# Performance work log

Measured on AMD Instinct MI355X. Metric: run time of the kernel, lower is better.

The kernel has to match this reference:

```python
import jax, jax.numpy as jnp
import numpy as np

EPS = 1e-5  # torch BatchNorm1d default eps
O, T, D, H1, H2 = 8, 4, 256, 64, 32


def setup_inputs() -> dict:
    key = jax.random.key(0)
    ks = jax.random.split(key, 8)
    B = 65536
    feature = jax.random.normal(ks[0], (B, D), dtype=jnp.float32)
    treatment = jax.random.randint(ks[1], (B,), 0, T, dtype=jnp.int64)
    s1 = 1.0 / np.sqrt(D)
    s2 = 1.0 / np.sqrt(H1)
    s3 = 1.0 / np.sqrt(H2)
    params = {
        # per (outcome, treatment) expert MLP weights
        'W1': jax.random.uniform(ks[2], (O, T, D, H1), jnp.float32, -s1, s1),
        'b1': jnp.zeros((O, T, H1), jnp.float32),
        'g1': jnp.ones((O, T, H1), jnp.float32),   # BN1 gamma
        'be1': jnp.zeros((O, T, H1), jnp.float32),  # BN1 beta
        'm1': jnp.zeros((O, T, H1), jnp.float32),   # BN1 running mean
        'v1': jnp.ones((O, T, H1), jnp.float32),    # BN1 running var
        'W2': jax.random.uniform(ks[3], (O, T, H1, H2), jnp.float32, -s2, s2),
        'b2': jnp.zeros((O, T, H2), jnp.float32),
        'g2': jnp.ones((O, T, H2), jnp.float32),
        'be2': jnp.zeros((O, T, H2), jnp.float32),
        'm2': jnp.zeros((O, T, H2), jnp.float32),
        'v2': jnp.ones((O, T, H2), jnp.float32),
        'W3': jax.random.uniform(ks[4], (O, T, H2), jnp.float32, -s3, s3),  # final Linear(32,1), squeezed
        'b3': jnp.zeros((O, T), jnp.float32),
    }
    return {'feature': feature, 'treatment': treatment, **params}


def _tlearner_fwd(x, t, W1, b1, g1, be1, m1, v1, W2, b2, g2, be2, m2, v2, W3, b3):
    # Dense evaluation of every (outcome, treatment) expert, then per-row
    # selection by treatment id. Equivalent (in eval mode: BN uses running
    # stats, dropout off) to the masked dispatch of the original module.
    h = jnp.einsum('bd,otdh->both', x, W1) + b1          # [B,O,T,H1]
    h = jax.nn.relu(h)
    h = (h - m1) * jax.lax.rsqrt(v1 + EPS) * g1 + be1    # BN1 (eval)
    h = jnp.einsum('both,othk->botk', h, W2) + b2        # [B,O,T,H2]
    h = jax.nn.relu(h)
    h = (h - m2) * jax.lax.rsqrt(v2 + EPS) * g2 + be2    # BN2 (eval)
    out = jnp.einsum('botk,otk->bot', h, W3) + b3        # [B,O,T]
    idx = t.astype(jnp.int32)[:, None, None]             # [B,1,1]
    return jnp.take_along_axis(out, jnp.broadcast_to(idx, (out.shape[0], O, 1)), axis=2)[..., 0]  # [B,O]


def reference(feature, treatment, W1, b1, g1, be1, m1, v1, W2, b2, g2, be2, m2, v2, W3, b3):
    return _tlearner_fwd(feature, treatment, W1, b1, g1, be1, m1, v1,
                         W2, b2, g2, be2, m2, v2, W3, b3)
```

## Files before the change

### kernel.cpp

```cpp
#include <hip/hip_runtime.h>
#include <cstdint>

typedef short bf16x8 __attribute__((ext_vector_type(8)));
typedef float f32x4 __attribute__((ext_vector_type(4)));

#define NO 8
#define NT 4
#define ND 256
#define NH1 64
#define NH2 32
#define BM 32
#define BNEPS 1e-5f

__device__ __forceinline__ unsigned bfpack2(float a, float b) {
    unsigned ua = __float_as_uint(a), ub = __float_as_uint(b);
    ua = (ua + 0x7FFFu + ((ua >> 16) & 1u)) >> 16;
    ub = (ub + 0x7FFFu + ((ub >> 16) & 1u)) >> 16;
    return ua | (ub << 16);
}


__global__ void k_hist_prep(const int* __restrict__ trt, int* __restrict__ ws, int B,
                            const float* __restrict__ W1, const float* __restrict__ W2,
                            const float* __restrict__ b1, const float* __restrict__ g1,
                            const float* __restrict__ be1, const float* __restrict__ m1,
                            const float* __restrict__ v1,
                            const float* __restrict__ b2, const float* __restrict__ g2,
                            const float* __restrict__ be2, const float* __restrict__ m2,
                            const float* __restrict__ v2, const float* __restrict__ W3,
                            unsigned* __restrict__ W1T4, unsigned* __restrict__ W2T4,
                            float* __restrict__ P1, float* __restrict__ P2) {
    const int bid = blockIdx.x, tid = threadIdx.x;
    if (bid < 256) {
        __shared__ int loc[NT];
        if (tid < NT) loc[tid] = 0;
        __syncthreads();
        const int i = bid * 256 + tid;
        if (i < B) atomicAdd(&loc[trt[i] & 3], 1);
        __syncthreads();
        if (tid < NT) atomicAdd(&ws[tid], loc[tid]);
    } else if (bid < 512) {
        const int gi = (bid - 256) * 256 + tid;
        const int lane = gi & 63, nt = (gi >> 6) & 31, c = (gi >> 11) & 7, t = gi >> 14;
        const int n16 = lane & 15, kg = lane >> 4;
        const int n = nt * 16 + n16, o = n >> 6, h = n & 63;
        const int k0 = c * 32 + kg * 8;
        const float* src = W1 + ((size_t)(o * NT + t) * ND + k0) * NH1 + h;
        float v[8];
#pragma unroll
        for (int j = 0; j < 8; ++j) v[j] = src[(size_t)j * NH1];
        uint4 q;
        q.x = bfpack2(v[0], v[1]); q.y = bfpack2(v[2], v[3]);
        q.z = bfpack2(v[4], v[5]); q.w = bfpack2(v[6], v[7]);
        ((uint4*)W1T4)[gi] = q;
    } else if (bid < 544) {
        const int gi = (bid - 512) * 256 + tid;
        const int m16 = gi & 15, kg = (gi >> 4) & 3, ks = (gi >> 6) & 1,
                  kt = (gi >> 7) & 1, o = (gi >> 8) & 7, t = gi >> 11;
        const int k2 = kt * 16 + m16, hb = ks * 32 + kg * 8;
        const float* src = W2 + ((size_t)(o * NT + t) * NH1 + hb) * NH2 + k2;
        float v[8];
#pragma unroll
        for (int j = 0; j < 8; ++j) v[j] = src[(size_t)j * NH2];
        uint4 q;
        q.x = bfpack2(v[0], v[1]); q.y = bfpack2(v[2], v[3]);
        q.z = bfpack2(v[4], v[5]); q.w = bfpack2(v[6], v[7]);
        ((uint4*)W2T4)[gi] = q;
    } else if (bid < 552) {
        const int gi = (bid - 544) * 256 + tid;
        const int t = gi >> 9, n = gi & 511;
        const int o = n >> 6, h = n & 63;
        const int idx = (o * NT + t) * NH1 + h;
        const float sc = g1[idx] * rsqrtf(v1[idx] + BNEPS);
        P1[gi] = sc;
        P1[2048 + gi] = be1[idx] - m1[idx] * sc;
        P1[4096 + gi] = b1[idx];
    } else {
        const int gi = (bid - 552) * 256 + tid;
        const int t = gi >> 8, q = gi & 255;
        const int o = q >> 5, k2 = q & 31;
        const int idx = (o * NT + t) * NH2 + k2;
        const float s = g2[idx] * rsqrtf(v2[idx] + BNEPS);
        const float w3 = W3[idx];
        P2[gi] = s * w3;
        P2[1024 + gi] = (be2[idx] - m2[idx] * s) * w3;
        P2[2048 + gi] = b2[idx];
    }
}

__global__ void k_scatter(const int* __restrict__ trt, int* __restrict__ ws,
                          int* __restrict__ perm, int B) {
    __shared__ int loc[NT], gb[NT];
    const int tid = threadIdx.x;
    if (tid < NT) loc[tid] = 0;
    __syncthreads();
    const int i = blockIdx.x * blockDim.x + tid;
    int tt = 0, pos = 0;
    if (i < B) { tt = trt[i] & 3; pos = atomicAdd(&loc[tt], 1); }
    __syncthreads();
    if (tid < NT) {
        const int c0 = ws[0], c1 = ws[1], c2 = ws[2];
        const int ub = tid == 0 ? 0 : tid == 1 ? c0 : tid == 2 ? c0 + c1 : c0 + c1 + c2;
        gb[tid] = ub + atomicAdd(&ws[4 + tid], loc[tid]);
    }
    __syncthreads();
    if (i < B) perm[gb[tt] + pos] = i;
}

__global__ __launch_bounds__(256, 3) void k_main(
    const float* __restrict__ X, const int* __restrict__ ws, const int* __restrict__ perm,
    const char* __restrict__ W1T, const char* __restrict__ W2T,
    const float* __restrict__ P1, const float* __restrict__ P2,
    const float* __restrict__ pb3, float* __restrict__ out)
{
    const int c0 = ws[0], c1 = ws[1], c2 = ws[2], c3 = ws[3];
    const int q0 = (c0 + 31) & ~31, q1 = (c1 + 31) & ~31, q2 = (c2 + 31) & ~31;
    const int e0 = q0, e1 = q0 + q1, e2 = e1 + q2, e3 = e2 + ((c3 + 31) & ~31);
    const int m0 = blockIdx.x * BM;
    if (m0 >= e3) return;
    const int t = (m0 >= e0) + (m0 >= e1) + (m0 >= e2);
    const int pb = t == 0 ? 0 : t == 1 ? e0 : t == 2 ? e1 : e2;
    const int ub = t == 0 ? 0 : t == 1 ? c0 : t == 2 ? c0 + c1 : c0 + c1 + c2;
    const int n_t = t == 0 ? c0 : t == 1 ? c1 : t == 2 ? c2 : c3;
    const int ploc0 = m0 - pb;

    const int tid = threadIdx.x;
    const int w = tid >> 6;
    const int l = tid & 63;

    __shared__ __align__(16) char LDS[32768];

    const int pl = ploc0 + (l & 31);
    const int rid_l = perm[ub + min(pl, n_t - 1)];

#pragma unroll
    for (int j = 0; j < 8; ++j) {
        const int r = w * 8 + j;
        const int rr = __shfl(rid_l, r);
        const float4 xv = *(const float4*)(X + (size_t)rr * ND + l * 4);
        uint2 pk;
        pk.x = bfpack2(xv.x, xv.y);
        pk.y = bfpack2(xv.z, xv.w);
        *(uint2*)(LDS + r * 512 + ((l * 8) ^ ((r & 7) << 4))) = pk;
    }

    f32x4 acc[8][2];
#pragma unroll
    for (int nt = 0; nt < 8; ++nt)
#pragma unroll
        for (int rt = 0; rt < 2; ++rt) acc[nt][rt] = (f32x4){0.f, 0.f, 0.f, 0.f};

    const char* W1Tt = W1T + (size_t)t * 262144;
    const int ln4 = (l >> 4) * 4;

    __syncthreads();

#pragma unroll
    for (int c = 0; c < 8; ++c) {
        bf16x8 aA[8];
#pragma unroll
        for (int nt = 0; nt < 8; ++nt)
            aA[nt] = *(const bf16x8*)(W1Tt + c * 32768 + (w * 8 + nt) * 1024 + l * 16);
#pragma unroll
        for (int rt = 0; rt < 2; ++rt) {
            const int r = rt * 16 + (l & 15);
            const bf16x8 bX = *(const bf16x8*)(LDS + r * 512 +
                                               ((c * 64 + (l >> 4) * 16) ^ ((r & 7) << 4)));
#pragma unroll
            for (int nt = 0; nt < 8; ++nt)
                acc[nt][rt] = __builtin_amdgcn_mfma_f32_16x16x32_bf16(aA[nt], bX, acc[nt][rt], 0, 0, 0);
        }
    }
    __syncthreads();

#pragma unroll
    for (int nt = 0; nt < 8; ++nt) {
        const int n0 = (w * 8 + nt) * 16 + ln4;
        const int p = t * 512 + n0;
        const float4 scv = *(const float4*)(P1 + p);
        const float4 shv = *(const float4*)(P1 + 2048 + p);
        const float4 bbv = *(const float4*)(P1 + 4096 + p);
#pragma unroll
        for (int rt = 0; rt < 2; ++rt) {
            const int r = rt * 16 + (l & 15);
            const f32x4 a = acc[nt][rt];
            const float z0 = fmaf(fmaxf(a[0] + bbv.x, 0.f), scv.x, shv.x);
            const float z1 = fmaf(fmaxf(a[1] + bbv.y, 0.f), scv.y, shv.y);
            const float z2 = fmaf(fmaxf(a[2] + bbv.z, 0.f), scv.z, shv.z);
            const float z3 = fmaf(fmaxf(a[3] + bbv.w, 0.f), scv.w, shv.w);
            uint2 pk;
            pk.x = bfpack2(z0, z1); pk.y = bfpack2(z2, z3);
            *(uint2*)(LDS + r * 1024 + (((unsigned)(n0 * 2)) ^ (unsigned)((r & 7) << 4))) = pk;
        }
    }

    bf16x8 aW[2][2][2];
#pragma unroll
    for (int oo = 0; oo < 2; ++oo) {
        const int o = w * 2 + oo;
#pragma unroll
        for (int kt = 0; kt < 2; ++kt)
#pragma unroll
            for (int ks = 0; ks < 2; ++ks)
                aW[oo][kt][ks] = *(const bf16x8*)(W2T +
                    ((((size_t)t * NO + o) * 2 + kt) * 2 + ks) * 1024 + l * 16);
    }
    f32x4 acc2[2][2][2];
#pragma unroll
    for (int oo = 0; oo < 2; ++oo)
#pragma unroll
        for (int kt = 0; kt < 2; ++kt)
#pragma unroll
            for (int rt2 = 0; rt2 < 2; ++rt2) acc2[oo][kt][rt2] = (f32x4){0.f, 0.f, 0.f, 0.f};

#pragma unroll
    for (int rt2 = 0; rt2 < 2; ++rt2) {
        const int r = rt2 * 16 + (l & 15);
        const unsigned swz = (unsigned)((r & 7) << 4);
#pragma unroll
        for (int ks = 0; ks < 2; ++ks) {
            const int nb = ks * 32 + (l >> 4) * 8;
#pragma unroll
            for (int oo = 0; oo < 2; ++oo) {
                const int n8 = (w * 2 + oo) * 64 + nb;
                const bf16x8 bH = *(const bf16x8*)(LDS + r * 1024 + (((unsigned)(n8 * 2)) ^ swz));
#pragma unroll
                for (int kt = 0; kt < 2; ++kt)
                    acc2[oo][kt][rt2] = __builtin_amdgcn_mfma_f32_16x16x32_bf16(aW[oo][kt][ks], bH, acc2[oo][kt][rt2], 0, 0, 0);
            }
        }
    }

    float p[2][2];
#pragma unroll
    for (int oo = 0; oo < 2; ++oo)
#pragma unroll
        for (int rt2 = 0; rt2 < 2; ++rt2) p[oo][rt2] = 0.f;

#pragma unroll
    for (int oo = 0; oo < 2; ++oo) {
        const int o = w * 2 + oo;
#pragma unroll
        for (int kt = 0; kt < 2; ++kt) {
            const int q = o * 32 + kt * 16 + ln4;
            const int p3 = t * 256 + q;
            const float4 A3 = *(const float4*)(P2 + p3);
            const float4 C3 = *(const float4*)(P2 + 1024 + p3);
            const float4 bb = *(const float4*)(P2 + 2048 + p3);
#pragma unroll
            for (int rt2 = 0; rt2 < 2; ++rt2) {
                const f32x4 a = acc2[oo][kt][rt2];
                float s = fmaf(fmaxf(a[0] + bb.x, 0.f), A3.x, C3.x);
                s = fmaf(fmaxf(a[1] + bb.y, 0.f), A3.y, s + C3.y);
                s = fmaf(fmaxf(a[2] + bb.z, 0.f), A3.z, s + C3.z);
                s = fmaf(fmaxf(a[3] + bb.w, 0.f), A3.w, s + C3.w);
                p[oo][rt2] += s;
            }
        }
    }
#pragma unroll
    for (int oo = 0; oo < 2; ++oo)
#pragma unroll
        for (int rt2 = 0; rt2 < 2; ++rt2) {
            float v = p[oo][rt2];
            v += __shfl_xor(v, 16);
            v += __shfl_xor(v, 32);
            p[oo][rt2] = v;
        }

    const int oo_s = l >> 5;
    const int rt2_s = (l >> 4) & 1;
    const int o_s = w * 2 + oo_s;
    const int r = rt2_s * 16 + (l & 15);
    const float v = oo_s ? (rt2_s ? p[1][1] : p[1][0]) : (rt2_s ? p[0][1] : p[0][0]);
    const int ra = __shfl(rid_l, r);
    if (ploc0 + r < n_t) out[(size_t)ra * NO + o_s] = v + pb3[o_s * NT + t];
}

extern "C" void kernel_launch(void* const* d_in, const int* in_sizes, int n_in,
                              void* d_out, int out_size, void* d_ws, size_t ws_size,
                              hipStream_t stream) {
    const float* X   = (const float*)d_in[0];
    const int* trt   = (const int*)d_in[1];
    const float* W1  = (const float*)d_in[2];
    const float* b1  = (const float*)d_in[3];
    const float* g1  = (const float*)d_in[4];
    const float* be1 = (const float*)d_in[5];
    const float* m1  = (const float*)d_in[6];
    const float* v1  = (const float*)d_in[7];
    const float* W2  = (const float*)d_in[8];
    const float* b2  = (const float*)d_in[9];
    const float* g2  = (const float*)d_in[10];
    const float* be2 = (const float*)d_in[11];
    const float* m2  = (const float*)d_in[12];
    const float* v2  = (const float*)d_in[13];
    const float* W3  = (const float*)d_in[14];
    const float* b3  = (const float*)d_in[15];
    float* out = (float*)d_out;

    const int B = in_sizes[1];
    int* wsi  = (int*)d_ws;
    int* perm = wsi + 16;
    char* wsb = (char*)d_ws;
    size_t off = (64 + (size_t)B * 4 + 15) & ~(size_t)15;
    char* W1T = wsb + off;
    char* W2T = W1T + 1048576;
    float* P1 = (float*)(W2T + 131072);
    float* P2 = P1 + 6144;

    hipMemsetAsync(wsi, 0, 64, stream);
    k_hist_prep<<<556, 256, 0, stream>>>(trt, wsi, B, W1, W2,
                                         b1, g1, be1, m1, v1,
                                         b2, g2, be2, m2, v2, W3,
                                         (unsigned*)W1T, (unsigned*)W2T, P1, P2);
    k_scatter<<<(B + 255) / 256, 256, 0, stream>>>(trt, wsi, perm, B);

    const int gx = (B + 31) / 32 + 4;
    k_main<<<gx, 256, 0, stream>>>(X, wsi, perm, W1T, W2T, P1, P2, b3, out);
}
```

Measured before the change: 61.82 us.

## Double row tile to 64 with 512-thread blocks and padded sentinel permutation

The main kernel now processes 64 rows per block with 8 waves. Each wave owns 4 hidden-column tiles across 4 row tiles in layer 1 and one outcome in layer 2, so each W1 fragment loaded from global feeds twice as many MFMAs. The scatter writes rows into per-treatment segments padded to 64, and the permutation is pre-filled with -1. Padding slots are clamped on load and skipped on store, which removes the per-row count bookkeeping. In exchange, LDS per block doubles, a second memset is added, and occupancy limits change.

```diff
diff --git a/kernel.cpp b/kernel.cpp
--- a/kernel.cpp
+++ b/kernel.cpp
@@ -9,7 +9,7 @@
 #define ND 256
 #define NH1 64
 #define NH2 32
-#define BM 32
+#define BM 64
 #define BNEPS 1e-5f
 
 __device__ __forceinline__ unsigned bfpack2(float a, float b) {
@@ -89,7 +89,7 @@
 }
 
 __global__ void k_scatter(const int* __restrict__ trt, int* __restrict__ ws,
-                          int* __restrict__ perm, int B) {
+                          int* __restrict__ rperm, int B) {
     __shared__ int loc[NT], gb[NT];
     const int tid = threadIdx.x;
     if (tid < NT) loc[tid] = 0;
@@ -100,90 +100,87 @@
     __syncthreads();
     if (tid < NT) {
         const int c0 = ws[0], c1 = ws[1], c2 = ws[2];
-        const int ub = tid == 0 ? 0 : tid == 1 ? c0 : tid == 2 ? c0 + c1 : c0 + c1 + c2;
-        gb[tid] = ub + atomicAdd(&ws[4 + tid], loc[tid]);
-    }
-    __syncthreads();
-    if (i < B) perm[gb[tt] + pos] = i;
-}
-
-__global__ __launch_bounds__(256, 3) void k_main(
-    const float* __restrict__ X, const int* __restrict__ ws, const int* __restrict__ perm,
+        const int q0 = (c0 + 63) & ~63, q1 = (c1 + 63) & ~63, q2 = (c2 + 63) & ~63;
+        const int eb = tid == 0 ? 0 : tid == 1 ? q0 : tid == 2 ? q0 + q1 : q0 + q1 + q2;
+        gb[tid] = eb + atomicAdd(&ws[4 + tid], loc[tid]);
+    }
+    __syncthreads();
+    if (i < B) rperm[gb[tt] + pos] = i;
+}
+
+__global__ __launch_bounds__(512, 2) void k_main(
+    const float* __restrict__ X, const int* __restrict__ ws, const int* __restrict__ rperm,
     const char* __restrict__ W1T, const char* __restrict__ W2T,
     const float* __restrict__ P1, const float* __restrict__ P2,
     const float* __restrict__ pb3, float* __restrict__ out)
 {
     const int c0 = ws[0], c1 = ws[1], c2 = ws[2], c3 = ws[3];
-    const int q0 = (c0 + 31) & ~31, q1 = (c1 + 31) & ~31, q2 = (c2 + 31) & ~31;
-    const int e0 = q0, e1 = q0 + q1, e2 = e1 + q2, e3 = e2 + ((c3 + 31) & ~31);
+    const int q0 = (c0 + 63) & ~63, q1 = (c1 + 63) & ~63, q2 = (c2 + 63) & ~63;
+    const int e0 = q0, e1 = q0 + q1, e2 = e1 + q2, e3 = e2 + ((c3 + 63) & ~63);
     const int m0 = blockIdx.x * BM;
     if (m0 >= e3) return;
     const int t = (m0 >= e0) + (m0 >= e1) + (m0 >= e2);
-    const int pb = t == 0 ? 0 : t == 1 ? e0 : t == 2 ? e1 : e2;
-    const int ub = t == 0 ? 0 : t == 1 ? c0 : t == 2 ? c0 + c1 : c0 + c1 + c2;
-    const int n_t = t == 0 ? c0 : t == 1 ? c1 : t == 2 ? c2 : c3;
-    const int ploc0 = m0 - pb;
 
     const int tid = threadIdx.x;
     const int w = tid >> 6;
     const int l = tid & 63;
 
-    __shared__ __align__(16) char LDS[32768];
-
-    const int pl = ploc0 + (l & 31);
-    const int rid_l = perm[ub + min(pl, n_t - 1)];
+    __shared__ __align__(16) char LDS[65536];
+
+    const int rid_l = rperm[m0 + l];
 
 #pragma unroll
     for (int j = 0; j < 8; ++j) {
         const int r = w * 8 + j;
         const int rr = __shfl(rid_l, r);
-        const float4 xv = *(const float4*)(X + (size_t)rr * ND + l * 4);
+        const int rrow = rr < 0 ? 0 : rr;
+        const float4 xv = *(const float4*)(X + (size_t)rrow * ND + l * 4);
         uint2 pk;
         pk.x = bfpack2(xv.x, xv.y);
         pk.y = bfpack2(xv.z, xv.w);
         *(uint2*)(LDS + r * 512 + ((l * 8) ^ ((r & 7) << 4))) = pk;
     }
 
-    f32x4 acc[8][2];
-#pragma unroll
-    for (int nt = 0; nt < 8; ++nt)
-#pragma unroll
-        for (int rt = 0; rt < 2; ++rt) acc[nt][rt] = (f32x4){0.f, 0.f, 0.f, 0.f};
-
-    const char* W1Tt = W1T + (size_t)t * 262144;
+    f32x4 acc[4][4];
+#pragma unroll
+    for (int jn = 0; jn < 4; ++jn)
+#pragma unroll
+        for (int rt = 0; rt < 4; ++rt) acc[jn][rt] = (f32x4){0.f, 0.f, 0.f, 0.f};
+
+    const char* W1Tw = W1T + (size_t)t * 262144 + (w * 4) * 1024 + l * 16;
     const int ln4 = (l >> 4) * 4;
 
     __syncthreads();
 
 #pragma unroll
     for (int c = 0; c < 8; ++c) {
-        bf16x8 aA[8];
-#pragma unroll
-        for (int nt = 0; nt < 8; ++nt)
-            aA[nt] = *(const bf16x8*)(W1Tt + c * 32768 + (w * 8 + nt) * 1024 + l * 16);
-#pragma unroll
-        for (int rt = 0; rt < 2; ++rt) {
+        bf16x8 aA[4];
+#pragma unroll
+        for (int jn = 0; jn < 4; ++jn)
+            aA[jn] = *(const bf16x8*)(W1Tw + c * 32768 + jn * 1024);
+#pragma unroll
+        for (int rt = 0; rt < 4; ++rt) {
             const int r = rt * 16 + (l & 15);
             const bf16x8 bX = *(const bf16x8*)(LDS + r * 512 +
                                                ((c * 64 + (l >> 4) * 16) ^ ((r & 7) << 4)));
 #pragma unroll
-            for (int nt = 0; nt < 8; ++nt)
-                acc[nt][rt] = __builtin_amdgcn_mfma_f32_16x16x32_bf16(aA[nt], bX, acc[nt][rt], 0, 0, 0);
-        }
-    }
-    __syncthreads();
-
-#pragma unroll
-    for (int nt = 0; nt < 8; ++nt) {
-        const int n0 = (w * 8 + nt) * 16 + ln4;
+            for (int jn = 0; jn < 4; ++jn)
+                acc[jn][rt] = __builtin_amdgcn_mfma_f32_16x16x32_bf16(aA[jn], bX, acc[jn][rt], 0, 0, 0);
+        }
+    }
+    __syncthreads();
+
+#pragma unroll
+    for (int jn = 0; jn < 4; ++jn) {
+        const int n0 = (w * 4 + jn) * 16 + ln4;
         const int p = t * 512 + n0;
         const float4 scv = *(const float4*)(P1 + p);
         const float4 shv = *(const float4*)(P1 + 2048 + p);
         const float4 bbv = *(const float4*)(P1 + 4096 + p);
 #pragma unroll
-        for (int rt = 0; rt < 2; ++rt) {
+        for (int rt = 0; rt < 4; ++rt) {
             const int r = rt * 16 + (l & 15);
-            const f32x4 a = acc[nt][rt];
+            const f32x4 a = acc[jn][rt];
             const float z0 = fmaf(fmaxf(a[0] + bbv.x, 0.f), scv.x, shv.x);
             const float z1 = fmaf(fmaxf(a[1] + bbv.y, 0.f), scv.y, shv.y);
             const float z2 = fmaf(fmaxf(a[2] + bbv.z, 0.f), scv.z, shv.z);
@@ -194,87 +191,66 @@
         }
     }
 
-    bf16x8 aW[2][2][2];
-#pragma unroll
-    for (int oo = 0; oo < 2; ++oo) {
-        const int o = w * 2 + oo;
-#pragma unroll
-        for (int kt = 0; kt < 2; ++kt)
-#pragma unroll
-            for (int ks = 0; ks < 2; ++ks)
-                aW[oo][kt][ks] = *(const bf16x8*)(W2T +
-                    ((((size_t)t * NO + o) * 2 + kt) * 2 + ks) * 1024 + l * 16);
-    }
-    f32x4 acc2[2][2][2];
-#pragma unroll
-    for (int oo = 0; oo < 2; ++oo)
-#pragma unroll
-        for (int kt = 0; kt < 2; ++kt)
-#pragma unroll
-            for (int rt2 = 0; rt2 < 2; ++rt2) acc2[oo][kt][rt2] = (f32x4){0.f, 0.f, 0.f, 0.f};
-
-#pragma unroll
-    for (int rt2 = 0; rt2 < 2; ++rt2) {
+    bf16x8 aW[2][2];
+#pragma unroll
+    for (int kt = 0; kt < 2; ++kt)
+#pragma unroll
+        for (int ks = 0; ks < 2; ++ks)
+            aW[kt][ks] = *(const bf16x8*)(W2T +
+                ((((size_t)t * NO + w) * 2 + kt) * 2 + ks) * 1024 + l * 16);
+
+    f32x4 acc2[2][4];
+#pragma unroll
+    for (int kt = 0; kt < 2; ++kt)
+#pragma unroll
+        for (int rt2 = 0; rt2 < 4; ++rt2) acc2[kt][rt2] = (f32x4){0.f, 0.f, 0.f, 0.f};
+
+#pragma unroll
+    for (int rt2 = 0; rt2 < 4; ++rt2) {
         const int r = rt2 * 16 + (l & 15);
         const unsigned swz = (unsigned)((r & 7) << 4);
 #pragma unroll
         for (int ks = 0; ks < 2; ++ks) {
-            const int nb = ks * 32 + (l >> 4) * 8;
-#pragma unroll
-            for (int oo = 0; oo < 2; ++oo) {
-                const int n8 = (w * 2 + oo) * 64 + nb;
-                const bf16x8 bH = *(const bf16x8*)(LDS + r * 1024 + (((unsigned)(n8 * 2)) ^ swz));
-#pragma unroll
-                for (int kt = 0; kt < 2; ++kt)
-                    acc2[oo][kt][rt2] = __builtin_amdgcn_mfma_f32_16x16x32_bf16(aW[oo][kt][ks], bH, acc2[oo][kt][rt2], 0, 0, 0);
-            }
-        }
-    }
-
-    float p[2][2];
-#pragma unroll
-    for (int oo = 0; oo < 2; ++oo)
-#pragma unroll
-        for (int rt2 = 0; rt2 < 2; ++rt2) p[oo][rt2] = 0.f;
-
-#pragma unroll
-    for (int oo = 0; oo < 2; ++oo) {
-        const int o = w * 2 + oo;
-#pragma unroll
-        for (int kt = 0; kt < 2; ++kt) {
-            const int q = o * 32 + kt * 16 + ln4;
-            const int p3 = t * 256 + q;
-            const float4 A3 = *(const float4*)(P2 + p3);
-            const float4 C3 = *(const float4*)(P2 + 1024 + p3);
-            const float4 bb = *(const float4*)(P2 + 2048 + p3);
-#pragma unroll
-            for (int rt2 = 0; rt2 < 2; ++rt2) {
-                const f32x4 a = acc2[oo][kt][rt2];
-                float s = fmaf(fmaxf(a[0] + bb.x, 0.f), A3.x, C3.x);
-                s = fmaf(fmaxf(a[1] + bb.y, 0.f), A3.y, s + C3.y);
-                s = fmaf(fmaxf(a[2] + bb.z, 0.f), A3.z, s + C3.z);
-                s = fmaf(fmaxf(a[3] + bb.w, 0.f), A3.w, s + C3.w);
-                p[oo][rt2] += s;
-            }
-        }
-    }
-#pragma unroll
-    for (int oo = 0; oo < 2; ++oo)
-#pragma unroll
-        for (int rt2 = 0; rt2 < 2; ++rt2) {
-            float v = p[oo][rt2];
-            v += __shfl_xor(v, 16);
-            v += __shfl_xor(v, 32);
-            p[oo][rt2] = v;
-        }
-
-    const int oo_s = l >> 5;
-    const int rt2_s = (l >> 4) & 1;
-    const int o_s = w * 2 + oo_s;
-    const int r = rt2_s * 16 + (l & 15);
-    const float v = oo_s ? (rt2_s ? p[1][1] : p[1][0]) : (rt2_s ? p[0][1] : p[0][0]);
-    const int ra = __shfl(rid_l, r);
-    if (ploc0 + r < n_t) out[(size_t)ra * NO + o_s] = v + pb3[o_s * NT + t];
+            const int n8 = w * 64 + ks * 32 + (l >> 4) * 8;
+            const bf16x8 bH = *(const bf16x8*)(LDS + r * 1024 + (((unsigned)(n8 * 2)) ^ swz));
+#pragma unroll
+            for (int kt = 0; kt < 2; ++kt)
+                acc2[kt][rt2] = __builtin_amdgcn_mfma_f32_16x16x32_bf16(aW[kt][ks], bH, acc2[kt][rt2], 0, 0, 0);
+        }
+    }
+
+    float pr[4];
+#pragma unroll
+    for (int rt2 = 0; rt2 < 4; ++rt2) pr[rt2] = 0.f;
+
+#pragma unroll
+    for (int kt = 0; kt < 2; ++kt) {
+        const int q3 = w * 32 + kt * 16 + ln4;
+        const int p3 = t * 256 + q3;
+        const float4 A3 = *(const float4*)(P2 + p3);
+        const float4 C3 = *(const float4*)(P2 + 1024 + p3);
+        const float4 bb = *(const float4*)(P2 + 2048 + p3);
+#pragma unroll
+        for (int rt2 = 0; rt2 < 4; ++rt2) {
+            const f32x4 a = acc2[kt][rt2];
+            float s = fmaf(fmaxf(a[0] + bb.x, 0.f), A3.x, C3.x);
+            s = fmaf(fmaxf(a[1] + bb.y, 0.f), A3.y, s + C3.y);
+            s = fmaf(fmaxf(a[2] + bb.z, 0.f), A3.z, s + C3.z);
+            s = fmaf(fmaxf(a[3] + bb.w, 0.f), A3.w, s + C3.w);
+            pr[rt2] += s;
+        }
+    }
+#pragma unroll
+    for (int rt2 = 0; rt2 < 4; ++rt2) {
+        float v = pr[rt2];
+        v += __shfl_xor(v, 16);
+        v += __shfl_xor(v, 32);
+        pr[rt2] = v;
+    }
+
+    const int sel = l >> 4;
+    const float v = sel == 0 ? pr[0] : sel == 1 ? pr[1] : sel == 2 ? pr[2] : pr[3];
+    if (rid_l >= 0) out[(size_t)rid_l * NO + w] = v + pb3[w * NT + t];
 }
 
 extern "C" void kernel_launch(void* const* d_in, const int* in_sizes, int n_in,
@@ -299,22 +275,25 @@
     float* out = (float*)d_out;
 
     const int B = in_sizes[1];
-    int* wsi  = (int*)d_ws;
-    int* perm = wsi + 16;
-    char* wsb = (char*)d_ws;
-    size_t off = (64 + (size_t)B * 4 + 15) & ~(size_t)15;
+    const int permCap = B + 4 * BM;
+    int* wsi   = (int*)d_ws;
+    int* rperm = wsi + 16;
+    char* wsb  = (char*)d_ws;
+    size_t off = (64 + (size_t)permCap * 4 + 15) & ~(size_t)15;
     char* W1T = wsb + off;
     char* W2T = W1T + 1048576;
     float* P1 = (float*)(W2T + 131072);
     float* P2 = P1 + 6144;
 
     hipMemsetAsync(wsi, 0, 64, stream);
+    hipMemsetAsync(rperm, 0xFF, (size_t)permCap * 4, stream);
+
     k_hist_prep<<<556, 256, 0, stream>>>(trt, wsi, B, W1, W2,
                                          b1, g1, be1, m1, v1,
                                          b2, g2, be2, m2, v2, W3,
                                          (unsigned*)W1T, (unsigned*)W2T, P1, P2);
-    k_scatter<<<(B + 255) / 256, 256, 0, stream>>>(trt, wsi, perm, B);
-
-    const int gx = (B + 31) / 32 + 4;
-    k_main<<<gx, 256, 0, stream>>>(X, wsi, perm, W1T, W2T, P1, P2, b3, out);
-}
+    k_scatter<<<(B + 255) / 256, 256, 0, stream>>>(trt, wsi, rperm, B);
+
+    const int gx = (B + 63) / 64 + 4;
+    k_main<<<gx, 512, 0, stream>>>(X, wsi, rperm, W1T, W2T, P1, P2, b3, out);
+}
```

Result: slower. 63.18 us (+2.2%).

## Load X rows straight into MFMA registers and pad permutation with sentinel rows

Applied to the files above, without the earlier changes.

The layer-1 X operand is now read straight from global memory into registers in MFMA B-fragment layout and converted with the hardware bf16 pack instruction. This replaces the LDS staging pass and its barriers. The permutation now holds padded, per-treatment 32-aligned slots pre-filled with -1, so the main kernel drops the count-based index math and masks stores by sentinel. Hidden activations go to per-wave LDS slices, and the launch_bounds occupancy hint is removed. The cost is an extra memset, strided gathers of 32-byte chunks per lane, and possibly different occupancy.

```diff
diff --git a/kernel.cpp b/kernel.cpp
--- a/kernel.cpp
+++ b/kernel.cpp
@@ -17,6 +17,12 @@
     ua = (ua + 0x7FFFu + ((ua >> 16) & 1u)) >> 16;
     ub = (ub + 0x7FFFu + ((ub >> 16) & 1u)) >> 16;
     return ua | (ub << 16);
+}
+
+__device__ __forceinline__ unsigned cvtpk(float lo, float hi) {
+    unsigned r;
+    asm("v_cvt_pk_bf16_f32 %0, %1, %2" : "=v"(r) : "v"(lo), "v"(hi));
+    return r;
 }
 
 
@@ -89,7 +95,7 @@
 }
 
 __global__ void k_scatter(const int* __restrict__ trt, int* __restrict__ ws,
-                          int* __restrict__ perm, int B) {
+                          int* __restrict__ rperm, int B) {
     __shared__ int loc[NT], gb[NT];
     const int tid = threadIdx.x;
     if (tid < NT) loc[tid] = 0;
@@ -100,15 +106,16 @@
     __syncthreads();
     if (tid < NT) {
         const int c0 = ws[0], c1 = ws[1], c2 = ws[2];
-        const int ub = tid == 0 ? 0 : tid == 1 ? c0 : tid == 2 ? c0 + c1 : c0 + c1 + c2;
-        gb[tid] = ub + atomicAdd(&ws[4 + tid], loc[tid]);
+        const int q0 = (c0 + 31) & ~31, q1 = (c1 + 31) & ~31, q2 = (c2 + 31) & ~31;
+        const int eb = tid == 0 ? 0 : tid == 1 ? q0 : tid == 2 ? q0 + q1 : q0 + q1 + q2;
+        gb[tid] = eb + atomicAdd(&ws[4 + tid], loc[tid]);
     }
     __syncthreads();
-    if (i < B) perm[gb[tt] + pos] = i;
-}
-
-__global__ __launch_bounds__(256, 3) void k_main(
-    const float* __restrict__ X, const int* __restrict__ ws, const int* __restrict__ perm,
+    if (i < B) rperm[gb[tt] + pos] = i;
+}
+
+__global__ void k_main(
+    const float* __restrict__ X, const int* __restrict__ ws, const int* __restrict__ rperm,
     const char* __restrict__ W1T, const char* __restrict__ W2T,
     const float* __restrict__ P1, const float* __restrict__ P2,
     const float* __restrict__ pb3, float* __restrict__ out)
@@ -119,30 +126,23 @@
     const int m0 = blockIdx.x * BM;
     if (m0 >= e3) return;
     const int t = (m0 >= e0) + (m0 >= e1) + (m0 >= e2);
-    const int pb = t == 0 ? 0 : t == 1 ? e0 : t == 2 ? e1 : e2;
-    const int ub = t == 0 ? 0 : t == 1 ? c0 : t == 2 ? c0 + c1 : c0 + c1 + c2;
-    const int n_t = t == 0 ? c0 : t == 1 ? c1 : t == 2 ? c2 : c3;
-    const int ploc0 = m0 - pb;
 
     const int tid = threadIdx.x;
     const int w = tid >> 6;
     const int l = tid & 63;
 
     __shared__ __align__(16) char LDS[32768];
-
-    const int pl = ploc0 + (l & 31);
-    const int rid_l = perm[ub + min(pl, n_t - 1)];
-
-#pragma unroll
-    for (int j = 0; j < 8; ++j) {
-        const int r = w * 8 + j;
-        const int rr = __shfl(rid_l, r);
-        const float4 xv = *(const float4*)(X + (size_t)rr * ND + l * 4);
-        uint2 pk;
-        pk.x = bfpack2(xv.x, xv.y);
-        pk.y = bfpack2(xv.z, xv.w);
-        *(uint2*)(LDS + r * 512 + ((l * 8) ^ ((r & 7) << 4))) = pk;
-    }
+    char* HR = LDS + w * 8192;
+
+    const int rid_o = rperm[m0 + (l & 31)];
+
+    const int r0 = __shfl(rid_o, l & 15);
+    const int r1 = __shfl(rid_o, 16 + (l & 15));
+    const float* px0 = X + (size_t)(r0 < 0 ? 0 : r0) * ND + (l >> 4) * 8;
+    const float* px1 = X + (size_t)(r1 < 0 ? 0 : r1) * ND + (l >> 4) * 8;
+
+    const char* W1Tw = W1T + (size_t)t * 262144 + (w * 8) * 1024 + l * 16;
+    const int ln4 = (l >> 4) * 4;
 
     f32x4 acc[8][2];
 #pragma unroll
@@ -150,32 +150,34 @@
 #pragma unroll
         for (int rt = 0; rt < 2; ++rt) acc[nt][rt] = (f32x4){0.f, 0.f, 0.f, 0.f};
 
-    const char* W1Tt = W1T + (size_t)t * 262144;
-    const int ln4 = (l >> 4) * 4;
-
-    __syncthreads();
-
 #pragma unroll
     for (int c = 0; c < 8; ++c) {
+        const float4 xa0 = *(const float4*)(px0 + c * 32);
+        const float4 xb0 = *(const float4*)(px0 + c * 32 + 4);
+        const float4 xa1 = *(const float4*)(px1 + c * 32);
+        const float4 xb1 = *(const float4*)(px1 + c * 32 + 4);
         bf16x8 aA[8];
 #pragma unroll
         for (int nt = 0; nt < 8; ++nt)
-            aA[nt] = *(const bf16x8*)(W1Tt + c * 32768 + (w * 8 + nt) * 1024 + l * 16);
-#pragma unroll
-        for (int rt = 0; rt < 2; ++rt) {
-            const int r = rt * 16 + (l & 15);
-            const bf16x8 bX = *(const bf16x8*)(LDS + r * 512 +
-                                               ((c * 64 + (l >> 4) * 16) ^ ((r & 7) << 4)));
-#pragma unroll
-            for (int nt = 0; nt < 8; ++nt)
-                acc[nt][rt] = __builtin_amdgcn_mfma_f32_16x16x32_bf16(aA[nt], bX, acc[nt][rt], 0, 0, 0);
-        }
-    }
-    __syncthreads();
+            aA[nt] = *(const bf16x8*)(W1Tw + c * 32768 + nt * 1024);
+        uint4 u0, u1;
+        u0.x = cvtpk(xa0.x, xa0.y); u0.y = cvtpk(xa0.z, xa0.w);
+        u0.z = cvtpk(xb0.x, xb0.y); u0.w = cvtpk(xb0.z, xb0.w);
+        u1.x = cvtpk(xa1.x, xa1.y); u1.y = cvtpk(xa1.z, xa1.w);
+        u1.z = cvtpk(xb1.x, xb1.y); u1.w = cvtpk(xb1.z, xb1.w);
+        const bf16x8 bX0 = __builtin_bit_cast(bf16x8, u0);
+        const bf16x8 bX1 = __builtin_bit_cast(bf16x8, u1);
+#pragma unroll
+        for (int nt = 0; nt < 8; ++nt) {
+            acc[nt][0] = __builtin_amdgcn_mfma_f32_16x16x32_bf16(aA[nt], bX0, acc[nt][0], 0, 0, 0);
+            acc[nt][1] = __builtin_amdgcn_mfma_f32_16x16x32_bf16(aA[nt], bX1, acc[nt][1], 0, 0, 0);
+        }
+    }
 
 #pragma unroll
     for (int nt = 0; nt < 8; ++nt) {
         const int n0 = (w * 8 + nt) * 16 + ln4;
+        const int n0l = nt * 16 + ln4;
         const int p = t * 512 + n0;
         const float4 scv = *(const float4*)(P1 + p);
         const float4 shv = *(const float4*)(P1 + 2048 + p);
@@ -189,8 +191,8 @@
             const float z2 = fmaf(fmaxf(a[2] + bbv.z, 0.f), scv.z, shv.z);
             const float z3 = fmaf(fmaxf(a[3] + bbv.w, 0.f), scv.w, shv.w);
             uint2 pk;
-            pk.x = bfpack2(z0, z1); pk.y = bfpack2(z2, z3);
-            *(uint2*)(LDS + r * 1024 + (((unsigned)(n0 * 2)) ^ (unsigned)((r & 7) << 4))) = pk;
+            pk.x = cvtpk(z0, z1); pk.y = cvtpk(z2, z3);
+            *(uint2*)(HR + r * 256 + (((unsigned)(n0l * 2)) ^ (unsigned)((r & 7) << 4))) = pk;
         }
     }
 
@@ -219,11 +221,10 @@
         const unsigned swz = (unsigned)((r & 7) << 4);
 #pragma unroll
         for (int ks = 0; ks < 2; ++ks) {
-            const int nb = ks * 32 + (l >> 4) * 8;
 #pragma unroll
             for (int oo = 0; oo < 2; ++oo) {
-                const int n8 = (w * 2 + oo) * 64 + nb;
-                const bf16x8 bH = *(const bf16x8*)(LDS + r * 1024 + (((unsigned)(n8 * 2)) ^ swz));
+                const int n8l = oo * 64 + ks * 32 + (l >> 4) * 8;
+                const bf16x8 bH = *(const bf16x8*)(HR + r * 256 + (((unsigned)(n8l * 2)) ^ swz));
 #pragma unroll
                 for (int kt = 0; kt < 2; ++kt)
                     acc2[oo][kt][rt2] = __builtin_amdgcn_mfma_f32_16x16x32_bf16(aW[oo][kt][ks], bH, acc2[oo][kt][rt2], 0, 0, 0);
@@ -273,8 +274,8 @@
     const int o_s = w * 2 + oo_s;
     const int r = rt2_s * 16 + (l & 15);
     const float v = oo_s ? (rt2_s ? p[1][1] : p[1][0]) : (rt2_s ? p[0][1] : p[0][0]);
-    const int ra = __shfl(rid_l, r);
-    if (ploc0 + r < n_t) out[(size_t)ra * NO + o_s] = v + pb3[o_s * NT + t];
+    const int ra = __shfl(rid_o, r);
+    if (ra >= 0) out[(size_t)ra * NO + o_s] = v + pb3[o_s * NT + t];
 }
 
 extern "C" void kernel_launch(void* const* d_in, const int* in_sizes, int n_in,
@@ -299,22 +300,25 @@
     float* out = (float*)d_out;
 
     const int B = in_sizes[1];
-    int* wsi  = (int*)d_ws;
-    int* perm = wsi + 16;
-    char* wsb = (char*)d_ws;
-    size_t off = (64 + (size_t)B * 4 + 15) & ~(size_t)15;
+    const int permCap = B + 128;
+    int* wsi   = (int*)d_ws;
+    int* rperm = wsi + 16;
+    char* wsb  = (char*)d_ws;
+    size_t off = (64 + (size_t)permCap * 4 + 15) & ~(size_t)15;
     char* W1T = wsb + off;
     char* W2T = W1T + 1048576;
     float* P1 = (float*)(W2T + 131072);
     float* P2 = P1 + 6144;
 
     hipMemsetAsync(wsi, 0, 64, stream);
+    hipMemsetAsync(rperm, 0xFF, (size_t)permCap * 4, stream);
+
     k_hist_prep<<<556, 256, 0, stream>>>(trt, wsi, B, W1, W2,
                                          b1, g1, be1, m1, v1,
                                          b2, g2, be2, m2, v2, W3,
                                          (unsigned*)W1T, (unsigned*)W2T, P1, P2);
-    k_scatter<<<(B + 255) / 256, 256, 0, stream>>>(trt, wsi, perm, B);
-
-    const int gx = (B + 31) / 32 + 4;
-    k_main<<<gx, 256, 0, stream>>>(X, wsi, perm, W1T, W2T, P1, P2, b3, out);
-}
+    k_scatter<<<(B + 255) / 256, 256, 0, stream>>>(trt, wsi, rperm, B);
+
+    const int gx = (B + 128) / 32;
+    k_main<<<gx, 256, 0, stream>>>(X, wsi, rperm, W1T, W2T, P1, P2, b3, out);
+}
```

After: 99.77 us. +61.4%, slower.
